# Performance work log

Hardware: AMD Instinct MI355X
Metric: run time of the kernel (lower is better)

## Reference

```python
import jax, jax.numpy as jnp
import numpy as np

DK = 64
DROPOUT_P = 0.1


def setup_inputs() -> dict:
    key = jax.random.key(0)
    kq, kk, kv, km = jax.random.split(key, 4)
    B, S, D = 16, 2048, 64
    q = jax.random.normal(kq, (B, S, D), dtype=jnp.float32)
    k = jax.random.normal(kk, (B, S, D), dtype=jnp.float32)
    v = jax.random.normal(kv, (B, S, D), dtype=jnp.float32)
    attn_mask = jax.random.randint(km, (S, S), 0, 2, dtype=jnp.int32)
    return {"q": q, "k": k, "v": v, "attn_mask": attn_mask}


def reference(q, k, v, attn_mask):
    # q = q / sqrt(dk)
    qs = q * (1.0 / np.sqrt(DK)).astype(np.float32)
    # dots: [B, S_q, S_k]
    dots = jnp.einsum("bqd,bkd->bqk", qs, k)
    # mask: 0 -> -inf, 1 -> 0 (additive)
    add_mask = jnp.where(attn_mask == 0, -jnp.inf, 0.0).astype(dots.dtype)
    dots = dots + add_mask  # broadcast [S,S] over batch
    attn = jax.nn.softmax(dots, axis=-1)
    # inverted dropout, train mode, fixed key for determinism
    keep = jax.random.bernoulli(jax.random.key(42), 1.0 - DROPOUT_P, attn.shape)
    attn = jnp.where(keep, attn * (1.0 / (1.0 - DROPOUT_P)), 0.0)
    out = jnp.einsum("bqk,bkd->bqd", attn, v)
    return out
```

## Files before the change

kernel.cpp:

```cpp
#include <hip/hip_runtime.h>

#define BATCH 16
#define SEQ   2048
#define DIM   64
#define NTHREADS 256
#define NROWS    (BATCH * SEQ)
#define OUTELEMS (NROWS * DIM)

typedef short bf16x8 __attribute__((ext_vector_type(8)));
typedef float f32x4 __attribute__((ext_vector_type(4)));

__device__ __forceinline__ int ldsoff(int row) {
  return row * 72 + 16 * (row >> 2);
}
#define LDS_SZ (64 * 72 + 16 * 16)

__device__ __forceinline__ unsigned tf_bits(unsigned f) {
  unsigned x0 = 0u;
  unsigned x1 = f;
  const unsigned ks1 = 42u;
  const unsigned ks2 = 0x1BD11BDAu ^ 42u;
  x1 += ks1;
#define TF_R(r) { x0 += x1; x1 = __builtin_amdgcn_alignbit(x1, x1, 32u - (r)); x1 ^= x0; }
  TF_R(13) TF_R(15) TF_R(26) TF_R(6)
  x0 += ks1; x1 += ks2 + 1u;
  TF_R(17) TF_R(29) TF_R(16) TF_R(24)
  x0 += ks2; x1 += 2u;
  TF_R(13) TF_R(15) TF_R(26) TF_R(6)
  x1 += ks1 + 3u;
  TF_R(17) TF_R(29) TF_R(16) TF_R(24)
  x0 += ks1; x1 += ks2 + 4u;
  TF_R(13) TF_R(15) TF_R(26) TF_R(6)
  x0 += ks2; x1 += 5u;
#undef TF_R
  return x0 ^ x1;
}
#define KEEP_THRESH 0xE6666600u

__device__ __forceinline__ unsigned pack_bf16x2(float lo, float hi) {
  const unsigned l = (__float_as_uint(lo) + 0x8000u) >> 16;
  const unsigned h = (__float_as_uint(hi) + 0x8000u) & 0xFFFF0000u;
  return h | l;
}

#define WS_KF 0
#define WS_VF 1048576
#define WS_L  2097152

__global__ __launch_bounds__(NTHREADS)
void convert_kv(const float* __restrict__ k, const float* __restrict__ v,
                unsigned* __restrict__ ws) {
  const unsigned gid = blockIdx.x * NTHREADS + threadIdx.x;
  const unsigned e = gid & 262143u;
  const int lane = e & 63;
  const int ks = (e >> 6) & 1, nt = (e >> 7) & 3, kt = (e >> 9) & 31, b = e >> 14;
  const int tx = lane & 15, quad = lane >> 4;
  uint4 wout;
  if (gid < 262144u) {
    const float* src = k + ((size_t)b * SEQ + kt * 64 + 4 * tx + nt) * DIM
                         + ks * 32 + quad * 8;
    const float4 f0 = *(const float4*)src;
    const float4 f1 = *(const float4*)(src + 4);
    wout.x = pack_bf16x2(f0.x, f0.y); wout.y = pack_bf16x2(f0.z, f0.w);
    wout.z = pack_bf16x2(f1.x, f1.y); wout.w = pack_bf16x2(f1.z, f1.w);
    *(uint4*)(ws + WS_KF + (size_t)e * 4) = wout;
  } else {
    const float* src = v + ((size_t)b * SEQ + kt * 64 + ks * 32 + quad * 8) * DIM
                         + nt * 16 + tx;
    const float a0 = src[0 * DIM], a1 = src[1 * DIM], a2 = src[2 * DIM], a3 = src[3 * DIM];
    const float a4 = src[4 * DIM], a5 = src[5 * DIM], a6 = src[6 * DIM], a7 = src[7 * DIM];
    wout.x = pack_bf16x2(a0, a1); wout.y = pack_bf16x2(a2, a3);
    wout.z = pack_bf16x2(a4, a5); wout.w = pack_bf16x2(a6, a7);
    *(uint4*)(ws + WS_VF + (size_t)e * 4) = wout;
  }
}

__global__ __launch_bounds__(NTHREADS, 4)
void attn_fwd(const float* __restrict__ q, const unsigned* __restrict__ ws,
              const int* __restrict__ mask, float* __restrict__ out,
              float* __restrict__ lsum) {
  __shared__ unsigned short PS[LDS_SZ];

  const int t    = threadIdx.x;
  const int w    = t >> 6;
  const int lane = t & 63;
  const int tx   = lane & 15;
  const int quad = lane >> 4;

  int bid = blockIdx.x;
  const int half = bid >> 9;
  bid &= 511;
  const int bb = bid >> 5;
  const int q0 = (bid & 31) * 64;
  const int qw = q0 + 16 * w;
  const int kt0 = half * 16;

  const float qscale = 0.125f * 1.44269504088896340736f;

  bf16x8 aq[2];
  {
    const float* qr = q + ((size_t)bb * SEQ + qw + tx) * DIM + quad * 8;
#pragma unroll
    for (int ks = 0; ks < 2; ++ks) {
      const float4 f0 = *(const float4*)(qr + ks * 32);
      const float4 f1 = *(const float4*)(qr + ks * 32 + 4);
      union { unsigned u[4]; bf16x8 v; } a;
      a.u[0] = pack_bf16x2(f0.x * qscale, f0.y * qscale);
      a.u[1] = pack_bf16x2(f0.z * qscale, f0.w * qscale);
      a.u[2] = pack_bf16x2(f1.x * qscale, f1.y * qscale);
      a.u[3] = pack_bf16x2(f1.z * qscale, f1.w * qscale);
      aq[ks] = a.v;
    }
  }

  float lrun[4] = {0.f, 0.f, 0.f, 0.f};
  f32x4 oacc[4];
#pragma unroll
  for (int nt = 0; nt < 4; ++nt) oacc[nt] = (f32x4){0.f, 0.f, 0.f, 0.f};

  const unsigned* kfb = ws + WS_KF + (size_t)(bb * 32) * 2048 + (size_t)lane * 4;
  const unsigned* vfb = ws + WS_VF + (size_t)(bb * 32) * 2048 + (size_t)lane * 4;
  const int* mbase = mask + (size_t)(qw + quad * 4) * SEQ + 4 * tx;
  const unsigned fbase0 = (unsigned)(bb * SEQ + qw + quad * 4) * (unsigned)SEQ
                          + (unsigned)(4 * tx);

#pragma unroll 1
  for (int kt = kt0; kt < kt0 + 16; ++kt) {
    const int k0 = kt * 64;

    int4 mv[4];
#pragma unroll
    for (int reg = 0; reg < 4; ++reg)
      mv[reg] = *(const int4*)(mbase + (size_t)reg * SEQ + k0);

    const unsigned* kfp = kfb + (size_t)kt * 2048;
    bf16x8 kf[4][2];
#pragma unroll
    for (int nt = 0; nt < 4; ++nt)
#pragma unroll
      for (int ks = 0; ks < 2; ++ks)
        kf[nt][ks] = *(const bf16x8*)(kfp + (nt * 2 + ks) * 256);

    f32x4 qk[4];
#pragma unroll
    for (int nt = 0; nt < 4; ++nt) {
      f32x4 c = (f32x4){0.f, 0.f, 0.f, 0.f};
#pragma unroll
      for (int ks = 0; ks < 2; ++ks)
        c = __builtin_amdgcn_mfma_f32_16x16x32_bf16(aq[ks], kf[nt][ks], c, 0, 0, 0);
      qk[nt] = c;
    }

    const unsigned* vfp = vfb + (size_t)kt * 2048;
    bf16x8 vf[4][2];
#pragma unroll
    for (int nt = 0; nt < 4; ++nt)
#pragma unroll
      for (int ks = 0; ks < 2; ++ks)
        vf[nt][ks] = *(const bf16x8*)(vfp + (nt * 2 + ks) * 256);

    const unsigned fb = fbase0 + (unsigned)k0;
#pragma unroll
    for (int reg = 0; reg < 4; ++reg) {
      const int* mreg = (const int*)&mv[reg];
      float pd[4];
      float ls = 0.0f;
#pragma unroll
      for (int nt = 0; nt < 4; ++nt) {
        const float s = mreg[nt] ? qk[nt][reg] : -1e30f;
        const float e = __builtin_amdgcn_exp2f(s);
        ls += e;
        const unsigned bits = tf_bits(fb + (unsigned)(reg * SEQ) + (unsigned)nt);
        pd[nt] = (bits < KEEP_THRESH) ? e : 0.0f;
      }
      lrun[reg] += ls;
      uint2 pw;
      pw.x = pack_bf16x2(pd[0], pd[1]);
      pw.y = pack_bf16x2(pd[2], pd[3]);
      *(uint2*)&PS[ldsoff(16 * w + quad * 4 + reg) + 4 * tx] = pw;
    }

#pragma unroll
    for (int ks = 0; ks < 2; ++ks) {
      const bf16x8 ap = *(const bf16x8*)&PS[ldsoff(16 * w + tx) + ks * 32 + quad * 8];
#pragma unroll
      for (int nt = 0; nt < 4; ++nt)
        oacc[nt] = __builtin_amdgcn_mfma_f32_16x16x32_bf16(ap, vf[nt][ks], oacc[nt], 0, 0, 0);
    }
  }

  float lred[4];
#pragma unroll
  for (int reg = 0; reg < 4; ++reg) {
    float ls = lrun[reg];
    ls += __shfl_xor(ls, 1);
    ls += __shfl_xor(ls, 2);
    ls += __shfl_xor(ls, 4);
    ls += __shfl_xor(ls, 8);
    lred[reg] = ls;
  }
  if (tx == 0) {
#pragma unroll
    for (int reg = 0; reg < 4; ++reg)
      atomicAdd(&lsum[bb * SEQ + qw + quad * 4 + reg], lred[reg]);
  }
  float* ob = out + ((size_t)bb * SEQ + qw) * DIM;
#pragma unroll
  for (int nt = 0; nt < 4; ++nt)
#pragma unroll
    for (int reg = 0; reg < 4; ++reg)
      atomicAdd(&ob[(size_t)(quad * 4 + reg) * DIM + nt * 16 + tx], oacc[nt][reg]);
}

__global__ __launch_bounds__(NTHREADS)
void combine(float* __restrict__ out, const float* __restrict__ lsum) {
  const int gid = blockIdx.x * NTHREADS + threadIdx.x;
  const int row = gid >> 6;
  out[gid] = out[gid] * (1.0f / (0.9f * lsum[row]));
}

extern "C" void kernel_launch(void* const* d_in, const int* in_sizes, int n_in,
                              void* d_out, int out_size, void* d_ws, size_t ws_size,
                              hipStream_t stream) {
  const float* q = (const float*)d_in[0];
  const float* k = (const float*)d_in[1];
  const float* v = (const float*)d_in[2];
  const int* mask = (const int*)d_in[3];
  float* out = (float*)d_out;
  unsigned* ws = (unsigned*)d_ws;

  hipMemsetAsync(out, 0, (size_t)out_size * 4, stream);
  hipMemsetAsync((float*)d_ws + WS_L, 0, (size_t)NROWS * 4, stream);
  hipLaunchKernelGGL(convert_kv, dim3(2048), dim3(NTHREADS), 0, stream, k, v, ws);
  hipLaunchKernelGGL(attn_fwd, dim3(1024), dim3(NTHREADS), 0, stream,
                     q, ws, mask, out, (float*)d_ws + WS_L);
  hipLaunchKernelGGL(combine, dim3(OUTELEMS / NTHREADS), dim3(NTHREADS), 0, stream,
                     out, (const float*)d_ws + WS_L);
}
```

Baseline: 243.1 us.

## Drop split-K atomics, software-pipeline PV matmul with double-buffered V fragments

Each block now processes the full key range instead of half, so the output is written directly with the normalization applied in-kernel. This removes both memsets, the atomic adds and the separate combine kernel. The loop is software-pipelined: the PV MFMA of the previous tile overlaps with K/V/mask loads and the QK MFMA of the current tile, using two V fragment buffers. P is also packed to bf16 by truncation via a perm instruction, and occupancy hint drops to 2, which halves the grid and may reduce parallelism and latency hiding.

```diff
diff --git a/kernel.cpp b/kernel.cpp
--- a/kernel.cpp
+++ b/kernel.cpp
@@ -42,10 +42,12 @@
   const unsigned h = (__float_as_uint(hi) + 0x8000u) & 0xFFFF0000u;
   return h | l;
 }
+__device__ __forceinline__ unsigned pack_trunc(float lo, float hi) {
+  return __builtin_amdgcn_perm(__float_as_uint(hi), __float_as_uint(lo), 0x07060302u);
+}
 
 #define WS_KF 0
 #define WS_VF 1048576
-#define WS_L  2097152
 
 __global__ __launch_bounds__(NTHREADS)
 void convert_kv(const float* __restrict__ k, const float* __restrict__ v,
@@ -75,10 +77,9 @@
   }
 }
 
-__global__ __launch_bounds__(NTHREADS, 4)
+__global__ __launch_bounds__(NTHREADS, 2)
 void attn_fwd(const float* __restrict__ q, const unsigned* __restrict__ ws,
-              const int* __restrict__ mask, float* __restrict__ out,
-              float* __restrict__ lsum) {
+              const int* __restrict__ mask, float* __restrict__ out) {
   __shared__ unsigned short PS[LDS_SZ];
 
   const int t    = threadIdx.x;
@@ -87,13 +88,9 @@
   const int tx   = lane & 15;
   const int quad = lane >> 4;
 
-  int bid = blockIdx.x;
-  const int half = bid >> 9;
-  bid &= 511;
-  const int bb = bid >> 5;
-  const int q0 = (bid & 31) * 64;
+  const int bb = blockIdx.x >> 5;
+  const int q0 = (blockIdx.x & 31) * 64;
   const int qw = q0 + 16 * w;
-  const int kt0 = half * 16;
 
   const float qscale = 0.125f * 1.44269504088896340736f;
 
@@ -124,23 +121,47 @@
   const unsigned fbase0 = (unsigned)(bb * SEQ + qw + quad * 4) * (unsigned)SEQ
                           + (unsigned)(4 * tx);
 
-#pragma unroll 1
-  for (int kt = kt0; kt < kt0 + 16; ++kt) {
-    const int k0 = kt * 64;
-
+  bf16x8 vfA[4][2], vfB[4][2];
+
+#define RNG_PWRITE(kt_, qk_)                                                   \
+  {                                                                            \
+    const unsigned fb = fbase0 + (unsigned)((kt_) * 64);                       \
+    _Pragma("unroll")                                                          \
+    for (int reg = 0; reg < 4; ++reg) {                                        \
+      const int* mreg = (const int*)&mv[reg];                                  \
+      float pd[4];                                                             \
+      float ls = 0.0f;                                                         \
+      _Pragma("unroll")                                                        \
+      for (int nt = 0; nt < 4; ++nt) {                                         \
+        const float s = mreg[nt] ? qk_[nt][reg] : -1e30f;                      \
+        const float e = __builtin_amdgcn_exp2f(s);                             \
+        ls += e;                                                               \
+        const unsigned bits = tf_bits(fb + (unsigned)(reg * SEQ) + (unsigned)nt); \
+        pd[nt] = (bits < KEEP_THRESH) ? e : 0.0f;                              \
+      }                                                                        \
+      lrun[reg] += ls;                                                         \
+      uint2 pw;                                                                \
+      pw.x = pack_trunc(pd[0], pd[1]);                                         \
+      pw.y = pack_trunc(pd[2], pd[3]);                                         \
+      *(uint2*)&PS[ldsoff(16 * w + quad * 4 + reg) + 4 * tx] = pw;             \
+    }                                                                          \
+  }
+
+  {
+    const unsigned* kfp = kfb;
+    const unsigned* vfp = vfb;
+    bf16x8 kf[4][2];
+#pragma unroll
+    for (int nt = 0; nt < 4; ++nt)
+#pragma unroll
+      for (int ks = 0; ks < 2; ++ks) {
+        kf[nt][ks]  = *(const bf16x8*)(kfp + (nt * 2 + ks) * 256);
+        vfA[nt][ks] = *(const bf16x8*)(vfp + (nt * 2 + ks) * 256);
+      }
     int4 mv[4];
 #pragma unroll
     for (int reg = 0; reg < 4; ++reg)
-      mv[reg] = *(const int4*)(mbase + (size_t)reg * SEQ + k0);
-
-    const unsigned* kfp = kfb + (size_t)kt * 2048;
-    bf16x8 kf[4][2];
-#pragma unroll
-    for (int nt = 0; nt < 4; ++nt)
-#pragma unroll
-      for (int ks = 0; ks < 2; ++ks)
-        kf[nt][ks] = *(const bf16x8*)(kfp + (nt * 2 + ks) * 256);
-
+      mv[reg] = *(const int4*)(mbase + (size_t)reg * SEQ);
     f32x4 qk[4];
 #pragma unroll
     for (int nt = 0; nt < 4; ++nt) {
@@ -150,46 +171,61 @@
         c = __builtin_amdgcn_mfma_f32_16x16x32_bf16(aq[ks], kf[nt][ks], c, 0, 0, 0);
       qk[nt] = c;
     }
-
-    const unsigned* vfp = vfb + (size_t)kt * 2048;
-    bf16x8 vf[4][2];
+    RNG_PWRITE(0, qk)
+  }
+
+#define BODY(kt_, prevV, curV)                                                 \
+  {                                                                            \
+    const unsigned* kfp = kfb + (size_t)(kt_) * 2048;                          \
+    const unsigned* vfp = vfb + (size_t)(kt_) * 2048;                          \
+    bf16x8 kf[4][2];                                                           \
+    _Pragma("unroll")                                                          \
+    for (int nt = 0; nt < 4; ++nt)                                             \
+      _Pragma("unroll")                                                        \
+      for (int ks = 0; ks < 2; ++ks) {                                         \
+        kf[nt][ks]   = *(const bf16x8*)(kfp + (nt * 2 + ks) * 256);            \
+        curV[nt][ks] = *(const bf16x8*)(vfp + (nt * 2 + ks) * 256);            \
+      }                                                                        \
+    int4 mv[4];                                                                \
+    _Pragma("unroll")                                                          \
+    for (int reg = 0; reg < 4; ++reg)                                          \
+      mv[reg] = *(const int4*)(mbase + (size_t)reg * SEQ + (kt_) * 64);        \
+    _Pragma("unroll")                                                          \
+    for (int ks = 0; ks < 2; ++ks) {                                           \
+      const bf16x8 ap = *(const bf16x8*)&PS[ldsoff(16 * w + tx) + ks * 32 + quad * 8]; \
+      _Pragma("unroll")                                                        \
+      for (int nt = 0; nt < 4; ++nt)                                           \
+        oacc[nt] = __builtin_amdgcn_mfma_f32_16x16x32_bf16(ap, prevV[nt][ks],  \
+                                                           oacc[nt], 0, 0, 0); \
+    }                                                                          \
+    f32x4 qk[4];                                                               \
+    _Pragma("unroll")                                                          \
+    for (int nt = 0; nt < 4; ++nt) {                                           \
+      f32x4 c = (f32x4){0.f, 0.f, 0.f, 0.f};                                   \
+      _Pragma("unroll")                                                        \
+      for (int ks = 0; ks < 2; ++ks)                                           \
+        c = __builtin_amdgcn_mfma_f32_16x16x32_bf16(aq[ks], kf[nt][ks], c, 0, 0, 0); \
+      qk[nt] = c;                                                              \
+    }                                                                          \
+    RNG_PWRITE(kt_, qk)                                                        \
+  }
+
+#pragma unroll 1
+  for (int kt = 1; kt < 31; kt += 2) {
+    BODY(kt, vfA, vfB)
+    BODY(kt + 1, vfB, vfA)
+  }
+  BODY(31, vfA, vfB)
+
+#pragma unroll
+  for (int ks = 0; ks < 2; ++ks) {
+    const bf16x8 ap = *(const bf16x8*)&PS[ldsoff(16 * w + tx) + ks * 32 + quad * 8];
 #pragma unroll
     for (int nt = 0; nt < 4; ++nt)
-#pragma unroll
-      for (int ks = 0; ks < 2; ++ks)
-        vf[nt][ks] = *(const bf16x8*)(vfp + (nt * 2 + ks) * 256);
-
-    const unsigned fb = fbase0 + (unsigned)k0;
-#pragma unroll
-    for (int reg = 0; reg < 4; ++reg) {
-      const int* mreg = (const int*)&mv[reg];
-      float pd[4];
-      float ls = 0.0f;
-#pragma unroll
-      for (int nt = 0; nt < 4; ++nt) {
-        const float s = mreg[nt] ? qk[nt][reg] : -1e30f;
-        const float e = __builtin_amdgcn_exp2f(s);
-        ls += e;
-        const unsigned bits = tf_bits(fb + (unsigned)(reg * SEQ) + (unsigned)nt);
-        pd[nt] = (bits < KEEP_THRESH) ? e : 0.0f;
-      }
-      lrun[reg] += ls;
-      uint2 pw;
-      pw.x = pack_bf16x2(pd[0], pd[1]);
-      pw.y = pack_bf16x2(pd[2], pd[3]);
-      *(uint2*)&PS[ldsoff(16 * w + quad * 4 + reg) + 4 * tx] = pw;
-    }
-
-#pragma unroll
-    for (int ks = 0; ks < 2; ++ks) {
-      const bf16x8 ap = *(const bf16x8*)&PS[ldsoff(16 * w + tx) + ks * 32 + quad * 8];
-#pragma unroll
-      for (int nt = 0; nt < 4; ++nt)
-        oacc[nt] = __builtin_amdgcn_mfma_f32_16x16x32_bf16(ap, vf[nt][ks], oacc[nt], 0, 0, 0);
-    }
-  }
-
-  float lred[4];
+      oacc[nt] = __builtin_amdgcn_mfma_f32_16x16x32_bf16(ap, vfB[nt][ks], oacc[nt], 0, 0, 0);
+  }
+
+  float linv[4];
 #pragma unroll
   for (int reg = 0; reg < 4; ++reg) {
     float ls = lrun[reg];
@@ -197,26 +233,14 @@
     ls += __shfl_xor(ls, 2);
     ls += __shfl_xor(ls, 4);
     ls += __shfl_xor(ls, 8);
-    lred[reg] = ls;
-  }
-  if (tx == 0) {
+    linv[reg] = (1.0f / 0.9f) / ls;
+  }
+  float* ob = out + ((size_t)bb * SEQ + qw) * DIM;
+#pragma unroll
+  for (int nt = 0; nt < 4; ++nt)
 #pragma unroll
     for (int reg = 0; reg < 4; ++reg)
-      atomicAdd(&lsum[bb * SEQ + qw + quad * 4 + reg], lred[reg]);
-  }
-  float* ob = out + ((size_t)bb * SEQ + qw) * DIM;
-#pragma unroll
-  for (int nt = 0; nt < 4; ++nt)
-#pragma unroll
-    for (int reg = 0; reg < 4; ++reg)
-      atomicAdd(&ob[(size_t)(quad * 4 + reg) * DIM + nt * 16 + tx], oacc[nt][reg]);
-}
-
-__global__ __launch_bounds__(NTHREADS)
-void combine(float* __restrict__ out, const float* __restrict__ lsum) {
-  const int gid = blockIdx.x * NTHREADS + threadIdx.x;
-  const int row = gid >> 6;
-  out[gid] = out[gid] * (1.0f / (0.9f * lsum[row]));
+      ob[(size_t)(quad * 4 + reg) * DIM + nt * 16 + tx] = oacc[nt][reg] * linv[reg];
 }
 
 extern "C" void kernel_launch(void* const* d_in, const int* in_sizes, int n_in,
@@ -229,11 +253,7 @@
   float* out = (float*)d_out;
   unsigned* ws = (unsigned*)d_ws;
 
-  hipMemsetAsync(out, 0, (size_t)out_size * 4, stream);
-  hipMemsetAsync((float*)d_ws + WS_L, 0, (size_t)NROWS * 4, stream);
   hipLaunchKernelGGL(convert_kv, dim3(2048), dim3(NTHREADS), 0, stream, k, v, ws);
-  hipLaunchKernelGGL(attn_fwd, dim3(1024), dim3(NTHREADS), 0, stream,
-                     q, ws, mask, out, (float*)d_ws + WS_L);
-  hipLaunchKernelGGL(combine, dim3(OUTELEMS / NTHREADS), dim3(NTHREADS), 0, stream,
-                     out, (const float*)d_ws + WS_L);
-}
+  hipLaunchKernelGGL(attn_fwd, dim3(512), dim3(NTHREADS), 0, stream,
+                     q, ws, mask, out);
+}
```

After: 231.1 us. -4.9%, faster.
